# Performance work log

Hardware: AMD Instinct MI355X
Metric: run time of the kernel (lower is better)

## Reference

```python
import jax, jax.numpy as jnp
import numpy as np
from jax import lax

TAGSET = 32
START = 30  # tag_to_ix[START_TAG]
STOP = 31   # tag_to_ix[STOP_TAG]
# tag 0 is PAD

def setup_inputs() -> dict:
    key = jax.random.key(0)
    k1, k2, k3, k4 = jax.random.split(key, 4)
    B, L, T = 1024, 512, TAGSET
    feats = jax.random.normal(k1, (B, L, T), jnp.float32)
    transitions = jax.random.normal(k2, (T, T), jnp.float32) * 0.1
    word_seq_lens = jax.random.randint(k4, (B,), 1, L + 1)  # in [1, L]
    raw_tags = jax.random.randint(k3, (B, L), 1, 30)  # real tags in [1,30)
    pos = jnp.arange(L)[None, :]
    tags = jnp.where(pos < word_seq_lens[:, None], raw_tags, 0)  # PAD=0 beyond length
    return {"feats": feats, "transitions": transitions, "tags": tags,
            "word_seq_lens": word_seq_lens}


def _crf_nll(feats, transitions, tags, word_seq_lens):
    B, L, T = feats.shape

    # ---- forward algorithm (partition function), forward_pred ----
    # all_scores[b,l,i,j] = transitions[i,j] + feats[b,l,j]  (never materialized)
    alpha0 = transitions[START][None, :] + feats[:, 0]  # (B,T)

    def step(alpha, feat_t):
        # alpha:(B,T) over 'from' tag i; score[b,i,j] = alpha[b,i]+trans[i,j]+feat_t[b,j]
        m = alpha[:, :, None] + transitions[None, :, :] + feat_t[:, None, :]
        new = jax.nn.logsumexp(m, axis=1)  # (B,T)
        return new, new

    feats_t = jnp.swapaxes(feats, 0, 1)  # (L,B,T)
    _, alphas_rest = lax.scan(step, alpha0, feats_t[1:])
    alphas = jnp.concatenate([alpha0[None], alphas_rest], axis=0)  # (L,B,T)

    last_alpha = alphas[word_seq_lens - 1, jnp.arange(B)]  # (B,T) at position len-1
    last_alpha = last_alpha + transitions[:, STOP][None, :]
    forward_score = jnp.sum(jax.nn.logsumexp(last_alpha, axis=1))

    # ---- gold score, forward_labeled ----
    # currentTagScores[b,l,i] = transitions[i, tags[b,l]] + feats[b,l,tags[b,l]]
    emit = jnp.take_along_axis(feats, tags[:, :, None], axis=2)[:, :, 0]  # (B,L)
    cur = transitions.T[tags] + emit[:, :, None]  # (B,L,T)

    begin = cur[:, 0, START]  # (B,)
    end_tag = jnp.take_along_axis(tags, word_seq_lens[:, None] - 1, axis=1)[:, 0]
    end = transitions[end_tag, STOP]  # (B,)
    middle = jnp.take_along_axis(cur[:, 1:, :], tags[:, :L - 1, None], axis=2)[:, :, 0]
    mask = (tags[:, 1:] != 0).astype(feats.dtype)
    gold_score = jnp.sum(begin) + jnp.sum(end) + jnp.sum(middle * mask)

    return forward_score - gold_score


def reference(feats, transitions, tags, word_seq_lens):
    return _crf_nll(feats, transitions, tags, word_seq_lens)
```

## Files before the change

### kernel.cpp

```cpp
#include <hip/hip_runtime.h>

#define NTAG 32
#define START 30
#define STOP 31
#define LOG2E 1.44269504088896340736f
#define LN2 0.69314718055994530942f

typedef float f2 __attribute__((ext_vector_type(2)));
typedef float f4 __attribute__((ext_vector_type(4)));

__device__ __forceinline__ float fexp2(float x) {
#if __has_builtin(__builtin_amdgcn_exp2f)
    return __builtin_amdgcn_exp2f(x);
#else
    return exp2f(x);
#endif
}
__device__ __forceinline__ float flog2(float x) {
#if __has_builtin(__builtin_amdgcn_logf)
    return __builtin_amdgcn_logf(x);
#else
    return log2f(x);
#endif
}

#define PKMUL(d, s, e) asm("v_pk_mul_f32 %0, %1, %2" : "=v"(d) : "v"(s), "v"(e))
#define PKFMA(d, s, e) asm("v_pk_fma_f32 %0, %1, %2, %0" : "+v"(d) : "v"(s), "v"(e))
#define PKADD(d, x, y) asm("v_pk_add_f32 %0, %1, %2" : "=v"(d) : "v"(x), "v"(y))

#define REPEAT16(M) \
    M(0) M(1) M(2) M(3) M(4) M(5) M(6) M(7) \
    M(8) M(9) M(10) M(11) M(12) M(13) M(14) M(15)

#define STEP_CORE(fraw_, PRE, RN) { \
    const float F_ = fexp2((fraw_) * LOG2E); \
    const float y_ = (PRE) ? (S * F_) : S; \
    *swr = y_; \
    asm volatile("" ::: "memory"); \
    const f4 Q0 = srd4[0], Q1 = srd4[1], Q2 = srd4[2], Q3 = srd4[3], \
             Q4 = srd4[4], Q5 = srd4[5], Q6 = srd4[6], Q7 = srd4[7]; \
    const f2 s0  = __builtin_shufflevector(Q0, Q0, 0, 1), s1  = __builtin_shufflevector(Q0, Q0, 2, 3); \
    const f2 s2  = __builtin_shufflevector(Q1, Q1, 0, 1), s3  = __builtin_shufflevector(Q1, Q1, 2, 3); \
    const f2 s4  = __builtin_shufflevector(Q2, Q2, 0, 1), s5  = __builtin_shufflevector(Q2, Q2, 2, 3); \
    const f2 s6  = __builtin_shufflevector(Q3, Q3, 0, 1), s7  = __builtin_shufflevector(Q3, Q3, 2, 3); \
    const f2 s8  = __builtin_shufflevector(Q4, Q4, 0, 1), s9  = __builtin_shufflevector(Q4, Q4, 2, 3); \
    const f2 s10 = __builtin_shufflevector(Q5, Q5, 0, 1), s11 = __builtin_shufflevector(Q5, Q5, 2, 3); \
    const f2 s12 = __builtin_shufflevector(Q6, Q6, 0, 1), s13 = __builtin_shufflevector(Q6, Q6, 2, 3); \
    const f2 s14 = __builtin_shufflevector(Q7, Q7, 0, 1), s15 = __builtin_shufflevector(Q7, Q7, 2, 3); \
    f2 a0, a1, a2, a3; \
    PKMUL(a0, s0,  E2_0);  PKMUL(a1, s1,  E2_1);  PKMUL(a2, s2,  E2_2);  PKMUL(a3, s3,  E2_3); \
    PKFMA(a0, s4,  E2_4);  PKFMA(a1, s5,  E2_5);  PKFMA(a2, s6,  E2_6);  PKFMA(a3, s7,  E2_7); \
    PKFMA(a0, s8,  E2_8);  PKFMA(a1, s9,  E2_9);  PKFMA(a2, s10, E2_10); PKFMA(a3, s11, E2_11); \
    PKFMA(a0, s12, E2_12); PKFMA(a1, s13, E2_13); PKFMA(a2, s14, E2_14); PKFMA(a3, s15, E2_15); \
    f2 t01, t23, tt; \
    PKADD(t01, a0, a1); PKADD(t23, a2, a3); PKADD(tt, t01, t23); \
    const float r_ = tt.x + tt.y; \
    S = (PRE) ? r_ : (r_ * F_); \
    if (RN) { \
        const int k_ = ((__float_as_int(Q0.x) >> 23) & 0xff) - 127; \
        S = __int_as_float(__float_as_int(S) - (k_ << 23)); \
        M2i += k_; } }

#define STEP_RELOAD_F(FS, tload, RN) { const float fraw_ = FS; \
    { const int tc_ = ((tload) < L - 1) ? (tload) : (L - 1); \
      FS = frow[tc_ * NTAG + j]; } \
    STEP_CORE(fraw_, 0, RN) }
#define STEP_RELOAD_B(FS, tload, RN) { const float fraw_ = FS; \
    { const int tc_ = ((tload) > 0) ? (tload) : 0; \
      FS = frow[tc_ * NTAG + j]; } \
    STEP_CORE(fraw_, 1, RN) }

#define STEP_NR_F(FS, RN) { const float fraw_ = FS; STEP_CORE(fraw_, 0, RN) }
#define STEP_NR_B(FS, RN) { const float fraw_ = FS; STEP_CORE(fraw_, 1, RN) }

#define PIN_E2 \
    asm volatile("" : "+v"(E2_0),  "+v"(E2_1),  "+v"(E2_2),  "+v"(E2_3), \
                      "+v"(E2_4),  "+v"(E2_5),  "+v"(E2_6),  "+v"(E2_7)); \
    asm volatile("" : "+v"(E2_8),  "+v"(E2_9),  "+v"(E2_10), "+v"(E2_11), \
                      "+v"(E2_12), "+v"(E2_13), "+v"(E2_14), "+v"(E2_15));

__global__ __launch_bounds__(768, 1) void crf_nll_kernel(
    const float* __restrict__ feats,
    const float* __restrict__ trans,
    const int*   __restrict__ tags,
    const int*   __restrict__ wsl,
    float* __restrict__ out, int B, int L)
{
    __shared__ float strans[NTAG * NTAG];
    __shared__ __align__(16) float sBC[8][NTAG];
    __shared__ float sRes[8][NTAG];
    __shared__ int   sM2[8];
    for (int i = threadIdx.x; i < NTAG * NTAG; i += 768) strans[i] = trans[i];
    __syncthreads();

    const int wave = threadIdx.x >> 6;
    const int lane = threadIdx.x & 63;

    if (wave < 8) {
        const int dir = wave >> 2;
        int b = blockIdx.x * 4 + (wave & 3);
        if (b >= B) b = B - 1;
        b = __builtin_amdgcn_readfirstlane(b);
        if (lane < 32) {
            const int j = lane;
            const int n = __builtin_amdgcn_readfirstlane(wsl[b]);
            const int h = (n + 1) >> 1;
            const float* __restrict__ frow = feats + (size_t)b * L * NTAG;
            float* const swr = &sBC[wave][j];
            const f4* const srd4 = (const f4*)&sBC[wave][0];
            float S;
            int M2i = 0;

            if (dir == 0) {
#define DECL_E2(k) f2 E2_##k = { fexp2(strans[(2*(k)) * NTAG + j] * LOG2E), \
                                 fexp2(strans[(2*(k)+1) * NTAG + j] * LOG2E) };
                REPEAT16(DECL_E2)
#undef DECL_E2
                S = fexp2((strans[START * NTAG + j] + frow[j]) * LOG2E);
#define LDF(t_) frow[(((t_) < L - 1) ? (t_) : (L - 1)) * NTAG + j]
                float fA0 = LDF(1),  fA1 = LDF(2),  fA2 = LDF(3),  fA3 = LDF(4),
                      fA4 = LDF(5),  fA5 = LDF(6),  fA6 = LDF(7),  fA7 = LDF(8);
                float fB0 = LDF(9),  fB1 = LDF(10), fB2 = LDF(11), fB3 = LDF(12),
                      fB4 = LDF(13), fB5 = LDF(14), fB6 = LDF(15), fB7 = LDF(16);
#undef LDF
                int t = 1;
                for (; t + 16 <= h; t += 16) {
                    PIN_E2
                    STEP_RELOAD_F(fA0, t + 16, 0)
                    STEP_RELOAD_F(fA1, t + 17, 0)
                    STEP_RELOAD_F(fA2, t + 18, 0)
                    STEP_RELOAD_F(fA3, t + 19, 1)
                    STEP_RELOAD_F(fA4, t + 20, 0)
                    STEP_RELOAD_F(fA5, t + 21, 0)
                    STEP_RELOAD_F(fA6, t + 22, 0)
                    STEP_RELOAD_F(fA7, t + 23, 1)
                    STEP_RELOAD_F(fB0, t + 24, 0)
                    STEP_RELOAD_F(fB1, t + 25, 0)
                    STEP_RELOAD_F(fB2, t + 26, 0)
                    STEP_RELOAD_F(fB3, t + 27, 1)
                    STEP_RELOAD_F(fB4, t + 28, 0)
                    STEP_RELOAD_F(fB5, t + 29, 0)
                    STEP_RELOAD_F(fB6, t + 30, 0)
                    STEP_RELOAD_F(fB7, t + 31, 1)
                }
                if (t + 0  < h) { STEP_NR_F(fA0, 1) }
                if (t + 1  < h) { STEP_NR_F(fA1, 1) }
                if (t + 2  < h) { STEP_NR_F(fA2, 1) }
                if (t + 3  < h) { STEP_NR_F(fA3, 1) }
                if (t + 4  < h) { STEP_NR_F(fA4, 1) }
                if (t + 5  < h) { STEP_NR_F(fA5, 1) }
                if (t + 6  < h) { STEP_NR_F(fA6, 1) }
                if (t + 7  < h) { STEP_NR_F(fA7, 1) }
                if (t + 8  < h) { STEP_NR_F(fB0, 1) }
                if (t + 9  < h) { STEP_NR_F(fB1, 1) }
                if (t + 10 < h) { STEP_NR_F(fB2, 1) }
                if (t + 11 < h) { STEP_NR_F(fB3, 1) }
                if (t + 12 < h) { STEP_NR_F(fB4, 1) }
                if (t + 13 < h) { STEP_NR_F(fB5, 1) }
                if (t + 14 < h) { STEP_NR_F(fB6, 1) }
            } else {
#define DECL_E2(k) f2 E2_##k = { fexp2(strans[j * NTAG + (2*(k))] * LOG2E), \
                                 fexp2(strans[j * NTAG + (2*(k)+1)] * LOG2E) };
                REPEAT16(DECL_E2)
#undef DECL_E2
                S = fexp2(strans[j * NTAG + STOP] * LOG2E);
                const int cnt = n - h;
#define LDB(s_) frow[(((n - 1 - (s_)) > 0) ? (n - 1 - (s_)) : 0) * NTAG + j]
                float gA0 = LDB(0),  gA1 = LDB(1),  gA2 = LDB(2),  gA3 = LDB(3),
                      gA4 = LDB(4),  gA5 = LDB(5),  gA6 = LDB(6),  gA7 = LDB(7);
                float gB0 = LDB(8),  gB1 = LDB(9),  gB2 = LDB(10), gB3 = LDB(11),
                      gB4 = LDB(12), gB5 = LDB(13), gB6 = LDB(14), gB7 = LDB(15);
#undef LDB
                int s = 0;
                for (; s + 16 <= cnt; s += 16) {
                    PIN_E2
                    STEP_RELOAD_B(gA0, n - 1 - (s + 0)  - 16, 0)
                    STEP_RELOAD_B(gA1, n - 1 - (s + 1)  - 16, 0)
                    STEP_RELOAD_B(gA2, n - 1 - (s + 2)  - 16, 0)
                    STEP_RELOAD_B(gA3, n - 1 - (s + 3)  - 16, 1)
                    STEP_RELOAD_B(gA4, n - 1 - (s + 4)  - 16, 0)
                    STEP_RELOAD_B(gA5, n - 1 - (s + 5)  - 16, 0)
                    STEP_RELOAD_B(gA6, n - 1 - (s + 6)  - 16, 0)
                    STEP_RELOAD_B(gA7, n - 1 - (s + 7)  - 16, 1)
                    STEP_RELOAD_B(gB0, n - 1 - (s + 8)  - 16, 0)
                    STEP_RELOAD_B(gB1, n - 1 - (s + 9)  - 16, 0)
                    STEP_RELOAD_B(gB2, n - 1 - (s + 10) - 16, 0)
                    STEP_RELOAD_B(gB3, n - 1 - (s + 11) - 16, 1)
                    STEP_RELOAD_B(gB4, n - 1 - (s + 12) - 16, 0)
                    STEP_RELOAD_B(gB5, n - 1 - (s + 13) - 16, 0)
                    STEP_RELOAD_B(gB6, n - 1 - (s + 14) - 16, 0)
                    STEP_RELOAD_B(gB7, n - 1 - (s + 15) - 16, 1)
                }
                if (s + 0  < cnt) { STEP_NR_B(gA0, 1) }
                if (s + 1  < cnt) { STEP_NR_B(gA1, 1) }
                if (s + 2  < cnt) { STEP_NR_B(gA2, 1) }
                if (s + 3  < cnt) { STEP_NR_B(gA3, 1) }
                if (s + 4  < cnt) { STEP_NR_B(gA4, 1) }
                if (s + 5  < cnt) { STEP_NR_B(gA5, 1) }
                if (s + 6  < cnt) { STEP_NR_B(gA6, 1) }
                if (s + 7  < cnt) { STEP_NR_B(gA7, 1) }
                if (s + 8  < cnt) { STEP_NR_B(gB0, 1) }
                if (s + 9  < cnt) { STEP_NR_B(gB1, 1) }
                if (s + 10 < cnt) { STEP_NR_B(gB2, 1) }
                if (s + 11 < cnt) { STEP_NR_B(gB3, 1) }
                if (s + 12 < cnt) { STEP_NR_B(gB4, 1) }
                if (s + 13 < cnt) { STEP_NR_B(gB5, 1) }
                if (s + 14 < cnt) { STEP_NR_B(gB6, 1) }
            }
            sRes[wave][j] = S;
            if (j == 0) sM2[wave] = M2i;
        }
    } else {
        int b = blockIdx.x * 4 + (wave - 8);
        if (b < B) {
            b = __builtin_amdgcn_readfirstlane(b);
            const int n = wsl[b];
            const float* __restrict__ frow = feats + (size_t)b * L * NTAG;
            const int*   __restrict__ trow = tags  + (size_t)b * L;
            float acc = 0.f;
            for (int tt = lane; tt < L; tt += 64) {
                const int tg = trow[tt];
                if (tt == 0) {
                    acc += strans[START * NTAG + tg] + frow[tg];
                } else if (tt < n) {
                    const int tgp = trow[tt - 1];
                    acc += strans[tgp * NTAG + tg] + frow[tt * NTAG + tg];
                }
                if (tt == n - 1) {
                    acc += strans[tg * NTAG + STOP];
                }
            }
#pragma unroll
            for (int k = 1; k < 64; k <<= 1) acc += __shfl_xor(acc, k, 64);
            if (lane == 0) atomicAdd(out, -acc);
        }
    }

    __syncthreads();

    if (wave < 4) {
        const int b = blockIdx.x * 4 + wave;
        if (b < B && lane < 32) {
            float ex = sRes[wave][lane] * sRes[wave + 4][lane];
#pragma unroll
            for (int k = 1; k < 32; k <<= 1) ex += __shfl_xor(ex, k, 32);
            if (lane == 0)
                atomicAdd(out, LN2 * ((float)(sM2[wave] + sM2[wave + 4]) + flog2(ex)));
        }
    }
}

extern "C" void kernel_launch(void* const* d_in, const int* in_sizes, int n_in,
                              void* d_out, int out_size, void* d_ws, size_t ws_size,
                              hipStream_t stream) {
    const float* feats = (const float*)d_in[0];
    const float* trans = (const float*)d_in[1];
    const int*   tags  = (const int*)d_in[2];
    const int*   wsl   = (const int*)d_in[3];
    float* out = (float*)d_out;

    const int B = in_sizes[3];
    const int L = in_sizes[2] / B;

    (void)hipMemsetAsync(out, 0, sizeof(float), stream);
    const int grid = (B + 3) / 4;
    crf_nll_kernel<<<grid, 768, 0, stream>>>(feats, trans, tags, wsl, out, B, L);
}
```

Measured before the change: 139.2 us.

## Split CRF recurrence contraction across both wave halves using permlane32 swap

Each recurrence step now uses all 64 lanes of a wave. Each half-wave computes a partial dot product over 16 of the 32 source tags, and the two partials are combined with v_permlane32_swap. This halves the per-lane FMA chain and LDS read width, at the cost of an extra cross-lane swap per step. Renormalisation now uses each lane's own exponent, so per-lane scale counters are stored and rescaled to a common maximum in the final reduction.

New measurement: 129.8 us. 6.7% less time.

```diff
diff --git a/kernel.cpp b/kernel.cpp
--- a/kernel.cpp
+++ b/kernel.cpp
@@ -24,40 +24,45 @@
 #endif
 }
 
+__device__ __forceinline__ void plswap(float &a, float &b) {
+#if __has_builtin(__builtin_amdgcn_permlane32_swap)
+    auto r = __builtin_amdgcn_permlane32_swap(__float_as_int(a), __float_as_int(b),
+                                              false, false);
+    a = __int_as_float(r[0]);
+    b = __int_as_float(r[1]);
+#else
+    asm volatile("v_permlane32_swap_b32 %0, %1" : "+v"(a), "+v"(b));
+#endif
+}
+
 #define PKMUL(d, s, e) asm("v_pk_mul_f32 %0, %1, %2" : "=v"(d) : "v"(s), "v"(e))
 #define PKFMA(d, s, e) asm("v_pk_fma_f32 %0, %1, %2, %0" : "+v"(d) : "v"(s), "v"(e))
 #define PKADD(d, x, y) asm("v_pk_add_f32 %0, %1, %2" : "=v"(d) : "v"(x), "v"(y))
 
-#define REPEAT16(M) \
-    M(0) M(1) M(2) M(3) M(4) M(5) M(6) M(7) \
-    M(8) M(9) M(10) M(11) M(12) M(13) M(14) M(15)
+#define REPEAT8(M) M(0) M(1) M(2) M(3) M(4) M(5) M(6) M(7)
 
 #define STEP_CORE(fraw_, PRE, RN) { \
     const float F_ = fexp2((fraw_) * LOG2E); \
     const float y_ = (PRE) ? (S * F_) : S; \
     *swr = y_; \
     asm volatile("" ::: "memory"); \
-    const f4 Q0 = srd4[0], Q1 = srd4[1], Q2 = srd4[2], Q3 = srd4[3], \
-             Q4 = srd4[4], Q5 = srd4[5], Q6 = srd4[6], Q7 = srd4[7]; \
-    const f2 s0  = __builtin_shufflevector(Q0, Q0, 0, 1), s1  = __builtin_shufflevector(Q0, Q0, 2, 3); \
-    const f2 s2  = __builtin_shufflevector(Q1, Q1, 0, 1), s3  = __builtin_shufflevector(Q1, Q1, 2, 3); \
-    const f2 s4  = __builtin_shufflevector(Q2, Q2, 0, 1), s5  = __builtin_shufflevector(Q2, Q2, 2, 3); \
-    const f2 s6  = __builtin_shufflevector(Q3, Q3, 0, 1), s7  = __builtin_shufflevector(Q3, Q3, 2, 3); \
-    const f2 s8  = __builtin_shufflevector(Q4, Q4, 0, 1), s9  = __builtin_shufflevector(Q4, Q4, 2, 3); \
-    const f2 s10 = __builtin_shufflevector(Q5, Q5, 0, 1), s11 = __builtin_shufflevector(Q5, Q5, 2, 3); \
-    const f2 s12 = __builtin_shufflevector(Q6, Q6, 0, 1), s13 = __builtin_shufflevector(Q6, Q6, 2, 3); \
-    const f2 s14 = __builtin_shufflevector(Q7, Q7, 0, 1), s15 = __builtin_shufflevector(Q7, Q7, 2, 3); \
+    const f4 Q0 = srd4[0], Q1 = srd4[1], Q2 = srd4[2], Q3 = srd4[3]; \
+    const f2 s0 = __builtin_shufflevector(Q0, Q0, 0, 1), s1 = __builtin_shufflevector(Q0, Q0, 2, 3); \
+    const f2 s2 = __builtin_shufflevector(Q1, Q1, 0, 1), s3 = __builtin_shufflevector(Q1, Q1, 2, 3); \
+    const f2 s4 = __builtin_shufflevector(Q2, Q2, 0, 1), s5 = __builtin_shufflevector(Q2, Q2, 2, 3); \
+    const f2 s6 = __builtin_shufflevector(Q3, Q3, 0, 1), s7 = __builtin_shufflevector(Q3, Q3, 2, 3); \
     f2 a0, a1, a2, a3; \
-    PKMUL(a0, s0,  E2_0);  PKMUL(a1, s1,  E2_1);  PKMUL(a2, s2,  E2_2);  PKMUL(a3, s3,  E2_3); \
-    PKFMA(a0, s4,  E2_4);  PKFMA(a1, s5,  E2_5);  PKFMA(a2, s6,  E2_6);  PKFMA(a3, s7,  E2_7); \
-    PKFMA(a0, s8,  E2_8);  PKFMA(a1, s9,  E2_9);  PKFMA(a2, s10, E2_10); PKFMA(a3, s11, E2_11); \
-    PKFMA(a0, s12, E2_12); PKFMA(a1, s13, E2_13); PKFMA(a2, s14, E2_14); PKFMA(a3, s15, E2_15); \
+    PKMUL(a0, s0, E2_0); PKMUL(a1, s1, E2_1); PKMUL(a2, s2, E2_2); PKMUL(a3, s3, E2_3); \
+    PKFMA(a0, s4, E2_4); PKFMA(a1, s5, E2_5); PKFMA(a2, s6, E2_6); PKFMA(a3, s7, E2_7); \
     f2 t01, t23, tt; \
     PKADD(t01, a0, a1); PKADD(t23, a2, a3); PKADD(tt, t01, t23); \
-    const float r_ = tt.x + tt.y; \
+    const float part_ = tt.x + tt.y; \
+    float px_ = part_, py_ = part_; \
+    plswap(px_, py_); \
+    const float r_ = px_ + py_; \
     S = (PRE) ? r_ : (r_ * F_); \
     if (RN) { \
-        const int k_ = ((__float_as_int(Q0.x) >> 23) & 0xff) - 127; \
+        const int k_ = ((__float_as_int(S) >> 23) & 0xff) - 127; \
         S = __int_as_float(__float_as_int(S) - (k_ << 23)); \
         M2i += k_; } }
 
@@ -74,10 +79,8 @@
 #define STEP_NR_B(FS, RN) { const float fraw_ = FS; STEP_CORE(fraw_, 1, RN) }
 
 #define PIN_E2 \
-    asm volatile("" : "+v"(E2_0),  "+v"(E2_1),  "+v"(E2_2),  "+v"(E2_3), \
-                      "+v"(E2_4),  "+v"(E2_5),  "+v"(E2_6),  "+v"(E2_7)); \
-    asm volatile("" : "+v"(E2_8),  "+v"(E2_9),  "+v"(E2_10), "+v"(E2_11), \
-                      "+v"(E2_12), "+v"(E2_13), "+v"(E2_14), "+v"(E2_15));
+    asm volatile("" : "+v"(E2_0), "+v"(E2_1), "+v"(E2_2), "+v"(E2_3), \
+                      "+v"(E2_4), "+v"(E2_5), "+v"(E2_6), "+v"(E2_7));
 
 __global__ __launch_bounds__(768, 1) void crf_nll_kernel(
     const float* __restrict__ feats,
@@ -87,9 +90,9 @@
     float* __restrict__ out, int B, int L)
 {
     __shared__ float strans[NTAG * NTAG];
-    __shared__ __align__(16) float sBC[8][NTAG];
+    __shared__ __align__(16) float sBC[8][104];
     __shared__ float sRes[8][NTAG];
-    __shared__ int   sM2[8];
+    __shared__ int   sM2[8][NTAG];
     for (int i = threadIdx.x; i < NTAG * NTAG; i += 768) strans[i] = trans[i];
     __syncthreads();
 
@@ -101,115 +104,115 @@
         int b = blockIdx.x * 4 + (wave & 3);
         if (b >= B) b = B - 1;
         b = __builtin_amdgcn_readfirstlane(b);
-        if (lane < 32) {
-            const int j = lane;
-            const int n = __builtin_amdgcn_readfirstlane(wsl[b]);
-            const int h = (n + 1) >> 1;
-            const float* __restrict__ frow = feats + (size_t)b * L * NTAG;
-            float* const swr = &sBC[wave][j];
-            const f4* const srd4 = (const f4*)&sBC[wave][0];
-            float S;
-            int M2i = 0;
-
-            if (dir == 0) {
-#define DECL_E2(k) f2 E2_##k = { fexp2(strans[(2*(k)) * NTAG + j] * LOG2E), \
-                                 fexp2(strans[(2*(k)+1) * NTAG + j] * LOG2E) };
-                REPEAT16(DECL_E2)
+        const int j = lane & 31;
+        const bool up = lane >= 32;
+        const int ib = up ? 16 : 0;
+        const int n = __builtin_amdgcn_readfirstlane(wsl[b]);
+        const int h = (n + 1) >> 1;
+        const float* __restrict__ frow = feats + (size_t)b * L * NTAG;
+
+        float* const swr = &sBC[wave][(up ? 68 : 0) + j];
+        const f4* const srd4 = (const f4*)&sBC[wave][up ? 16 : 0];
+        float S;
+        int M2i = 0;
+
+        if (dir == 0) {
+#define DECL_E2(k) f2 E2_##k = { fexp2(strans[(ib + 2*(k)) * NTAG + j] * LOG2E), \
+                                 fexp2(strans[(ib + 2*(k) + 1) * NTAG + j] * LOG2E) };
+            REPEAT8(DECL_E2)
 #undef DECL_E2
-                S = fexp2((strans[START * NTAG + j] + frow[j]) * LOG2E);
+            S = fexp2((strans[START * NTAG + j] + frow[j]) * LOG2E);
 #define LDF(t_) frow[(((t_) < L - 1) ? (t_) : (L - 1)) * NTAG + j]
-                float fA0 = LDF(1),  fA1 = LDF(2),  fA2 = LDF(3),  fA3 = LDF(4),
-                      fA4 = LDF(5),  fA5 = LDF(6),  fA6 = LDF(7),  fA7 = LDF(8);
-                float fB0 = LDF(9),  fB1 = LDF(10), fB2 = LDF(11), fB3 = LDF(12),
-                      fB4 = LDF(13), fB5 = LDF(14), fB6 = LDF(15), fB7 = LDF(16);
+            float fA0 = LDF(1),  fA1 = LDF(2),  fA2 = LDF(3),  fA3 = LDF(4),
+                  fA4 = LDF(5),  fA5 = LDF(6),  fA6 = LDF(7),  fA7 = LDF(8);
+            float fB0 = LDF(9),  fB1 = LDF(10), fB2 = LDF(11), fB3 = LDF(12),
+                  fB4 = LDF(13), fB5 = LDF(14), fB6 = LDF(15), fB7 = LDF(16);
 #undef LDF
-                int t = 1;
-                for (; t + 16 <= h; t += 16) {
-                    PIN_E2
-                    STEP_RELOAD_F(fA0, t + 16, 0)
-                    STEP_RELOAD_F(fA1, t + 17, 0)
-                    STEP_RELOAD_F(fA2, t + 18, 0)
-                    STEP_RELOAD_F(fA3, t + 19, 1)
-                    STEP_RELOAD_F(fA4, t + 20, 0)
-                    STEP_RELOAD_F(fA5, t + 21, 0)
-                    STEP_RELOAD_F(fA6, t + 22, 0)
-                    STEP_RELOAD_F(fA7, t + 23, 1)
-                    STEP_RELOAD_F(fB0, t + 24, 0)
-                    STEP_RELOAD_F(fB1, t + 25, 0)
-                    STEP_RELOAD_F(fB2, t + 26, 0)
-                    STEP_RELOAD_F(fB3, t + 27, 1)
-                    STEP_RELOAD_F(fB4, t + 28, 0)
-                    STEP_RELOAD_F(fB5, t + 29, 0)
-                    STEP_RELOAD_F(fB6, t + 30, 0)
-                    STEP_RELOAD_F(fB7, t + 31, 1)
-                }
-                if (t + 0  < h) { STEP_NR_F(fA0, 1) }
-                if (t + 1  < h) { STEP_NR_F(fA1, 1) }
-                if (t + 2  < h) { STEP_NR_F(fA2, 1) }
-                if (t + 3  < h) { STEP_NR_F(fA3, 1) }
-                if (t + 4  < h) { STEP_NR_F(fA4, 1) }
-                if (t + 5  < h) { STEP_NR_F(fA5, 1) }
-                if (t + 6  < h) { STEP_NR_F(fA6, 1) }
-                if (t + 7  < h) { STEP_NR_F(fA7, 1) }
-                if (t + 8  < h) { STEP_NR_F(fB0, 1) }
-                if (t + 9  < h) { STEP_NR_F(fB1, 1) }
-                if (t + 10 < h) { STEP_NR_F(fB2, 1) }
-                if (t + 11 < h) { STEP_NR_F(fB3, 1) }
-                if (t + 12 < h) { STEP_NR_F(fB4, 1) }
-                if (t + 13 < h) { STEP_NR_F(fB5, 1) }
-                if (t + 14 < h) { STEP_NR_F(fB6, 1) }
-            } else {
-#define DECL_E2(k) f2 E2_##k = { fexp2(strans[j * NTAG + (2*(k))] * LOG2E), \
-                                 fexp2(strans[j * NTAG + (2*(k)+1)] * LOG2E) };
-                REPEAT16(DECL_E2)
+            int t = 1;
+            for (; t + 16 <= h; t += 16) {
+                PIN_E2
+                STEP_RELOAD_F(fA0, t + 16, 0)
+                STEP_RELOAD_F(fA1, t + 17, 0)
+                STEP_RELOAD_F(fA2, t + 18, 0)
+                STEP_RELOAD_F(fA3, t + 19, 1)
+                STEP_RELOAD_F(fA4, t + 20, 0)
+                STEP_RELOAD_F(fA5, t + 21, 0)
+                STEP_RELOAD_F(fA6, t + 22, 0)
+                STEP_RELOAD_F(fA7, t + 23, 1)
+                STEP_RELOAD_F(fB0, t + 24, 0)
+                STEP_RELOAD_F(fB1, t + 25, 0)
+                STEP_RELOAD_F(fB2, t + 26, 0)
+                STEP_RELOAD_F(fB3, t + 27, 1)
+                STEP_RELOAD_F(fB4, t + 28, 0)
+                STEP_RELOAD_F(fB5, t + 29, 0)
+                STEP_RELOAD_F(fB6, t + 30, 0)
+                STEP_RELOAD_F(fB7, t + 31, 1)
+            }
+            if (t + 0  < h) { STEP_NR_F(fA0, 1) }
+            if (t + 1  < h) { STEP_NR_F(fA1, 1) }
+            if (t + 2  < h) { STEP_NR_F(fA2, 1) }
+            if (t + 3  < h) { STEP_NR_F(fA3, 1) }
+            if (t + 4  < h) { STEP_NR_F(fA4, 1) }
+            if (t + 5  < h) { STEP_NR_F(fA5, 1) }
+            if (t + 6  < h) { STEP_NR_F(fA6, 1) }
+            if (t + 7  < h) { STEP_NR_F(fA7, 1) }
+            if (t + 8  < h) { STEP_NR_F(fB0, 1) }
+            if (t + 9  < h) { STEP_NR_F(fB1, 1) }
+            if (t + 10 < h) { STEP_NR_F(fB2, 1) }
+            if (t + 11 < h) { STEP_NR_F(fB3, 1) }
+            if (t + 12 < h) { STEP_NR_F(fB4, 1) }
+            if (t + 13 < h) { STEP_NR_F(fB5, 1) }
+            if (t + 14 < h) { STEP_NR_F(fB6, 1) }
+        } else {
+#define DECL_E2(k) f2 E2_##k = { fexp2(strans[j * NTAG + ib + 2*(k)] * LOG2E), \
+                                 fexp2(strans[j * NTAG + ib + 2*(k) + 1] * LOG2E) };
+            REPEAT8(DECL_E2)
 #undef DECL_E2
-                S = fexp2(strans[j * NTAG + STOP] * LOG2E);
-                const int cnt = n - h;
+            S = fexp2(strans[j * NTAG + STOP] * LOG2E);
+            const int cnt = n - h;
 #define LDB(s_) frow[(((n - 1 - (s_)) > 0) ? (n - 1 - (s_)) : 0) * NTAG + j]
-                float gA0 = LDB(0),  gA1 = LDB(1),  gA2 = LDB(2),  gA3 = LDB(3),
-                      gA4 = LDB(4),  gA5 = LDB(5),  gA6 = LDB(6),  gA7 = LDB(7);
-                float gB0 = LDB(8),  gB1 = LDB(9),  gB2 = LDB(10), gB3 = LDB(11),
-                      gB4 = LDB(12), gB5 = LDB(13), gB6 = LDB(14), gB7 = LDB(15);
+            float gA0 = LDB(0),  gA1 = LDB(1),  gA2 = LDB(2),  gA3 = LDB(3),
+                  gA4 = LDB(4),  gA5 = LDB(5),  gA6 = LDB(6),  gA7 = LDB(7);
+            float gB0 = LDB(8),  gB1 = LDB(9),  gB2 = LDB(10), gB3 = LDB(11),
+                  gB4 = LDB(12), gB5 = LDB(13), gB6 = LDB(14), gB7 = LDB(15);
 #undef LDB
-                int s = 0;
-                for (; s + 16 <= cnt; s += 16) {
-                    PIN_E2
-                    STEP_RELOAD_B(gA0, n - 1 - (s + 0)  - 16, 0)
-                    STEP_RELOAD_B(gA1, n - 1 - (s + 1)  - 16, 0)
-                    STEP_RELOAD_B(gA2, n - 1 - (s + 2)  - 16, 0)
-                    STEP_RELOAD_B(gA3, n - 1 - (s + 3)  - 16, 1)
-                    STEP_RELOAD_B(gA4, n - 1 - (s + 4)  - 16, 0)
-                    STEP_RELOAD_B(gA5, n - 1 - (s + 5)  - 16, 0)
-                    STEP_RELOAD_B(gA6, n - 1 - (s + 6)  - 16, 0)
-                    STEP_RELOAD_B(gA7, n - 1 - (s + 7)  - 16, 1)
-                    STEP_RELOAD_B(gB0, n - 1 - (s + 8)  - 16, 0)
-                    STEP_RELOAD_B(gB1, n - 1 - (s + 9)  - 16, 0)
-                    STEP_RELOAD_B(gB2, n - 1 - (s + 10) - 16, 0)
-                    STEP_RELOAD_B(gB3, n - 1 - (s + 11) - 16, 1)
-                    STEP_RELOAD_B(gB4, n - 1 - (s + 12) - 16, 0)
-                    STEP_RELOAD_B(gB5, n - 1 - (s + 13) - 16, 0)
-                    STEP_RELOAD_B(gB6, n - 1 - (s + 14) - 16, 0)
-                    STEP_RELOAD_B(gB7, n - 1 - (s + 15) - 16, 1)
-                }
-                if (s + 0  < cnt) { STEP_NR_B(gA0, 1) }
-                if (s + 1  < cnt) { STEP_NR_B(gA1, 1) }
-                if (s + 2  < cnt) { STEP_NR_B(gA2, 1) }
-                if (s + 3  < cnt) { STEP_NR_B(gA3, 1) }
-                if (s + 4  < cnt) { STEP_NR_B(gA4, 1) }
-                if (s + 5  < cnt) { STEP_NR_B(gA5, 1) }
-                if (s + 6  < cnt) { STEP_NR_B(gA6, 1) }
-                if (s + 7  < cnt) { STEP_NR_B(gA7, 1) }
-                if (s + 8  < cnt) { STEP_NR_B(gB0, 1) }
-                if (s + 9  < cnt) { STEP_NR_B(gB1, 1) }
-                if (s + 10 < cnt) { STEP_NR_B(gB2, 1) }
-                if (s + 11 < cnt) { STEP_NR_B(gB3, 1) }
-                if (s + 12 < cnt) { STEP_NR_B(gB4, 1) }
-                if (s + 13 < cnt) { STEP_NR_B(gB5, 1) }
-                if (s + 14 < cnt) { STEP_NR_B(gB6, 1) }
-            }
-            sRes[wave][j] = S;
-            if (j == 0) sM2[wave] = M2i;
+            int s = 0;
+            for (; s + 16 <= cnt; s += 16) {
+                PIN_E2
+                STEP_RELOAD_B(gA0, n - 1 - (s + 0)  - 16, 0)
+                STEP_RELOAD_B(gA1, n - 1 - (s + 1)  - 16, 0)
+                STEP_RELOAD_B(gA2, n - 1 - (s + 2)  - 16, 0)
+                STEP_RELOAD_B(gA3, n - 1 - (s + 3)  - 16, 1)
+                STEP_RELOAD_B(gA4, n - 1 - (s + 4)  - 16, 0)
+                STEP_RELOAD_B(gA5, n - 1 - (s + 5)  - 16, 0)
+                STEP_RELOAD_B(gA6, n - 1 - (s + 6)  - 16, 0)
+                STEP_RELOAD_B(gA7, n - 1 - (s + 7)  - 16, 1)
+                STEP_RELOAD_B(gB0, n - 1 - (s + 8)  - 16, 0)
+                STEP_RELOAD_B(gB1, n - 1 - (s + 9)  - 16, 0)
+                STEP_RELOAD_B(gB2, n - 1 - (s + 10) - 16, 0)
+                STEP_RELOAD_B(gB3, n - 1 - (s + 11) - 16, 1)
+                STEP_RELOAD_B(gB4, n - 1 - (s + 12) - 16, 0)
+                STEP_RELOAD_B(gB5, n - 1 - (s + 13) - 16, 0)
+                STEP_RELOAD_B(gB6, n - 1 - (s + 14) - 16, 0)
+                STEP_RELOAD_B(gB7, n - 1 - (s + 15) - 16, 1)
+            }
+            if (s + 0  < cnt) { STEP_NR_B(gA0, 1) }
+            if (s + 1  < cnt) { STEP_NR_B(gA1, 1) }
+            if (s + 2  < cnt) { STEP_NR_B(gA2, 1) }
+            if (s + 3  < cnt) { STEP_NR_B(gA3, 1) }
+            if (s + 4  < cnt) { STEP_NR_B(gA4, 1) }
+            if (s + 5  < cnt) { STEP_NR_B(gA5, 1) }
+            if (s + 6  < cnt) { STEP_NR_B(gA6, 1) }
+            if (s + 7  < cnt) { STEP_NR_B(gA7, 1) }
+            if (s + 8  < cnt) { STEP_NR_B(gB0, 1) }
+            if (s + 9  < cnt) { STEP_NR_B(gB1, 1) }
+            if (s + 10 < cnt) { STEP_NR_B(gB2, 1) }
+            if (s + 11 < cnt) { STEP_NR_B(gB3, 1) }
+            if (s + 12 < cnt) { STEP_NR_B(gB4, 1) }
+            if (s + 13 < cnt) { STEP_NR_B(gB5, 1) }
+            if (s + 14 < cnt) { STEP_NR_B(gB6, 1) }
         }
+        if (!up) { sRes[wave][j] = S; sM2[wave][j] = M2i; }
     } else {
         int b = blockIdx.x * 4 + (wave - 8);
         if (b < B) {
@@ -239,13 +242,21 @@
     __syncthreads();
 
     if (wave < 4) {
-        const int b = blockIdx.x * 4 + wave;
-        if (b < B && lane < 32) {
-            float ex = sRes[wave][lane] * sRes[wave + 4][lane];
+        const int b2 = blockIdx.x * 4 + wave;
+        if (b2 < B && lane < 32) {
+            const int M2s = sM2[wave][lane] + sM2[wave + 4][lane];
+            const float pr = sRes[wave][lane] * sRes[wave + 4][lane];
+            int mx = M2s;
+#pragma unroll
+            for (int k = 1; k < 32; k <<= 1) {
+                const int o = __shfl_xor(mx, k, 32);
+                mx = o > mx ? o : mx;
+            }
+            float ex = ldexpf(pr, M2s - mx);
 #pragma unroll
             for (int k = 1; k < 32; k <<= 1) ex += __shfl_xor(ex, k, 32);
             if (lane == 0)
-                atomicAdd(out, LN2 * ((float)(sM2[wave] + sM2[wave + 4]) + flog2(ex)));
+                atomicAdd(out, LN2 * ((float)mx + flog2(ex)));
         }
     }
 }
```

## Pack forward and backward CRF recursions into one wave's two half-waves

Applied to the files above, without the earlier changes.

The forward and backward CRF recursions for a sequence now run in the lower and upper 32 lanes of a single wave instead of two separate half-idle waves, so the block shrinks from 12 to 8 waves. The two halves are combined with a permlane32 swap plus shuffle reduction, which removes the trailing __syncthreads and shared-memory exchange. Loads now use a precomputed byte offset stepped each iteration, and the tail is a fixed 16-step predicated epilogue instead of branches. The forward and backward step counts can differ by one, so the main loop is bounded by the forward count and per-lane predication covers the rest, adding divergence-free but redundant work in the epilogue.

After: 139.7 us. No clear change (+0.4%).

```diff
diff --git a/kernel.cpp b/kernel.cpp
--- a/kernel.cpp
+++ b/kernel.cpp
@@ -24,6 +24,25 @@
 #endif
 }
 
+__device__ __forceinline__ void plswapf(float &a, float &b) {
+#if __has_builtin(__builtin_amdgcn_permlane32_swap)
+    auto r = __builtin_amdgcn_permlane32_swap(__float_as_int(a), __float_as_int(b),
+                                              false, false);
+    a = __int_as_float(r[0]);
+    b = __int_as_float(r[1]);
+#else
+    asm volatile("s_nop 1\n\tv_permlane32_swap_b32 %0, %1" : "+v"(a), "+v"(b));
+#endif
+}
+__device__ __forceinline__ void plswapi(int &a, int &b) {
+#if __has_builtin(__builtin_amdgcn_permlane32_swap)
+    auto r = __builtin_amdgcn_permlane32_swap(a, b, false, false);
+    a = r[0]; b = r[1];
+#else
+    asm volatile("s_nop 1\n\tv_permlane32_swap_b32 %0, %1" : "+v"(a), "+v"(b));
+#endif
+}
+
 #define PKMUL(d, s, e) asm("v_pk_mul_f32 %0, %1, %2" : "=v"(d) : "v"(s), "v"(e))
 #define PKFMA(d, s, e) asm("v_pk_fma_f32 %0, %1, %2, %0" : "+v"(d) : "v"(s), "v"(e))
 #define PKADD(d, x, y) asm("v_pk_add_f32 %0, %1, %2" : "=v"(d) : "v"(x), "v"(y))
@@ -32,9 +51,10 @@
     M(0) M(1) M(2) M(3) M(4) M(5) M(6) M(7) \
     M(8) M(9) M(10) M(11) M(12) M(13) M(14) M(15)
 
-#define STEP_CORE(fraw_, PRE, RN) { \
+#define STEP_CORE(fraw_, RN, ACT) { \
     const float F_ = fexp2((fraw_) * LOG2E); \
-    const float y_ = (PRE) ? (S * F_) : S; \
+    const float SF_ = S * F_; \
+    const float y_ = up ? SF_ : S; \
     *swr = y_; \
     asm volatile("" ::: "memory"); \
     const f4 Q0 = srd4[0], Q1 = srd4[1], Q2 = srd4[2], Q3 = srd4[3], \
@@ -55,23 +75,21 @@
     f2 t01, t23, tt; \
     PKADD(t01, a0, a1); PKADD(t23, a2, a3); PKADD(tt, t01, t23); \
     const float r_ = tt.x + tt.y; \
-    S = (PRE) ? r_ : (r_ * F_); \
+    const float rF_ = r_ * F_; \
+    const float val_ = up ? r_ : rF_; \
+    S = (ACT) ? val_ : S; \
     if (RN) { \
         const int k_ = ((__float_as_int(Q0.x) >> 23) & 0xff) - 127; \
         S = __int_as_float(__float_as_int(S) - (k_ << 23)); \
         M2i += k_; } }
 
-#define STEP_RELOAD_F(FS, tload, RN) { const float fraw_ = FS; \
-    { const int tc_ = ((tload) < L - 1) ? (tload) : (L - 1); \
-      FS = frow[tc_ * NTAG + j]; } \
-    STEP_CORE(fraw_, 0, RN) }
-#define STEP_RELOAD_B(FS, tload, RN) { const float fraw_ = FS; \
-    { const int tc_ = ((tload) > 0) ? (tload) : 0; \
-      FS = frow[tc_ * NTAG + j]; } \
-    STEP_CORE(fraw_, 1, RN) }
-
-#define STEP_NR_F(FS, RN) { const float fraw_ = FS; STEP_CORE(fraw_, 0, RN) }
-#define STEP_NR_B(FS, RN) { const float fraw_ = FS; STEP_CORE(fraw_, 1, RN) }
+#define STEP_RELOAD(FS, RN) { const float fraw_ = FS; \
+    { FS = *(const float*)((const char*)frow + (voff + d16)); voff += dStep; } \
+    STEP_CORE(fraw_, RN, 1) }
+
+#define STEP_EP(FS, i_) { const float fraw_ = FS; \
+    const bool act_ = (i_) < rl; \
+    STEP_CORE(fraw_, 1, act_) }
 
 #define PIN_E2 \
     asm volatile("" : "+v"(E2_0),  "+v"(E2_1),  "+v"(E2_2),  "+v"(E2_3), \
@@ -79,7 +97,7 @@
     asm volatile("" : "+v"(E2_8),  "+v"(E2_9),  "+v"(E2_10), "+v"(E2_11), \
                       "+v"(E2_12), "+v"(E2_13), "+v"(E2_14), "+v"(E2_15));
 
-__global__ __launch_bounds__(768, 1) void crf_nll_kernel(
+__global__ __launch_bounds__(512, 1) void crf_nll_kernel(
     const float* __restrict__ feats,
     const float* __restrict__ trans,
     const int*   __restrict__ tags,
@@ -87,131 +105,105 @@
     float* __restrict__ out, int B, int L)
 {
     __shared__ float strans[NTAG * NTAG];
-    __shared__ __align__(16) float sBC[8][NTAG];
-    __shared__ float sRes[8][NTAG];
-    __shared__ int   sM2[8];
-    for (int i = threadIdx.x; i < NTAG * NTAG; i += 768) strans[i] = trans[i];
+    __shared__ __align__(16) float sBC[4][2][NTAG];
+    for (int i = threadIdx.x; i < NTAG * NTAG; i += 512) strans[i] = trans[i];
     __syncthreads();
 
     const int wave = threadIdx.x >> 6;
     const int lane = threadIdx.x & 63;
 
-    if (wave < 8) {
-        const int dir = wave >> 2;
-        int b = blockIdx.x * 4 + (wave & 3);
-        if (b >= B) b = B - 1;
+    if (wave < 4) {
+        int b = blockIdx.x * 4 + wave;
+        const int bok = (b < B);
+        if (!bok) b = B - 1;
         b = __builtin_amdgcn_readfirstlane(b);
-        if (lane < 32) {
-            const int j = lane;
-            const int n = __builtin_amdgcn_readfirstlane(wsl[b]);
-            const int h = (n + 1) >> 1;
-            const float* __restrict__ frow = feats + (size_t)b * L * NTAG;
-            float* const swr = &sBC[wave][j];
-            const f4* const srd4 = (const f4*)&sBC[wave][0];
-            float S;
-            int M2i = 0;
-
-            if (dir == 0) {
-#define DECL_E2(k) f2 E2_##k = { fexp2(strans[(2*(k)) * NTAG + j] * LOG2E), \
-                                 fexp2(strans[(2*(k)+1) * NTAG + j] * LOG2E) };
-                REPEAT16(DECL_E2)
+
+        const int j = lane & 31;
+        const bool up = lane >= 32;
+        const int n = __builtin_amdgcn_readfirstlane(wsl[b]);
+        const int h = (n + 1) >> 1;
+        const int cf = h - 1;
+        const int cb = n - h;
+        const int climit = up ? cb : cf;
+        const float* __restrict__ frow = feats + (size_t)b * L * NTAG;
+
+#define DECL_E2(k) f2 E2_##k = { \
+        fexp2(strans[up ? (j * NTAG + 2*(k))     : ((2*(k)) * NTAG + j)]     * LOG2E), \
+        fexp2(strans[up ? (j * NTAG + 2*(k) + 1) : ((2*(k)+1) * NTAG + j)] * LOG2E) };
+        REPEAT16(DECL_E2)
 #undef DECL_E2
-                S = fexp2((strans[START * NTAG + j] + frow[j]) * LOG2E);
-#define LDF(t_) frow[(((t_) < L - 1) ? (t_) : (L - 1)) * NTAG + j]
-                float fA0 = LDF(1),  fA1 = LDF(2),  fA2 = LDF(3),  fA3 = LDF(4),
-                      fA4 = LDF(5),  fA5 = LDF(6),  fA6 = LDF(7),  fA7 = LDF(8);
-                float fB0 = LDF(9),  fB1 = LDF(10), fB2 = LDF(11), fB3 = LDF(12),
-                      fB4 = LDF(13), fB5 = LDF(14), fB6 = LDF(15), fB7 = LDF(16);
-#undef LDF
-                int t = 1;
-                for (; t + 16 <= h; t += 16) {
-                    PIN_E2
-                    STEP_RELOAD_F(fA0, t + 16, 0)
-                    STEP_RELOAD_F(fA1, t + 17, 0)
-                    STEP_RELOAD_F(fA2, t + 18, 0)
-                    STEP_RELOAD_F(fA3, t + 19, 1)
-                    STEP_RELOAD_F(fA4, t + 20, 0)
-                    STEP_RELOAD_F(fA5, t + 21, 0)
-                    STEP_RELOAD_F(fA6, t + 22, 0)
-                    STEP_RELOAD_F(fA7, t + 23, 1)
-                    STEP_RELOAD_F(fB0, t + 24, 0)
-                    STEP_RELOAD_F(fB1, t + 25, 0)
-                    STEP_RELOAD_F(fB2, t + 26, 0)
-                    STEP_RELOAD_F(fB3, t + 27, 1)
-                    STEP_RELOAD_F(fB4, t + 28, 0)
-                    STEP_RELOAD_F(fB5, t + 29, 0)
-                    STEP_RELOAD_F(fB6, t + 30, 0)
-                    STEP_RELOAD_F(fB7, t + 31, 1)
-                }
-                if (t + 0  < h) { STEP_NR_F(fA0, 1) }
-                if (t + 1  < h) { STEP_NR_F(fA1, 1) }
-                if (t + 2  < h) { STEP_NR_F(fA2, 1) }
-                if (t + 3  < h) { STEP_NR_F(fA3, 1) }
-                if (t + 4  < h) { STEP_NR_F(fA4, 1) }
-                if (t + 5  < h) { STEP_NR_F(fA5, 1) }
-                if (t + 6  < h) { STEP_NR_F(fA6, 1) }
-                if (t + 7  < h) { STEP_NR_F(fA7, 1) }
-                if (t + 8  < h) { STEP_NR_F(fB0, 1) }
-                if (t + 9  < h) { STEP_NR_F(fB1, 1) }
-                if (t + 10 < h) { STEP_NR_F(fB2, 1) }
-                if (t + 11 < h) { STEP_NR_F(fB3, 1) }
-                if (t + 12 < h) { STEP_NR_F(fB4, 1) }
-                if (t + 13 < h) { STEP_NR_F(fB5, 1) }
-                if (t + 14 < h) { STEP_NR_F(fB6, 1) }
-            } else {
-#define DECL_E2(k) f2 E2_##k = { fexp2(strans[j * NTAG + (2*(k))] * LOG2E), \
-                                 fexp2(strans[j * NTAG + (2*(k)+1)] * LOG2E) };
-                REPEAT16(DECL_E2)
-#undef DECL_E2
-                S = fexp2(strans[j * NTAG + STOP] * LOG2E);
-                const int cnt = n - h;
-#define LDB(s_) frow[(((n - 1 - (s_)) > 0) ? (n - 1 - (s_)) : 0) * NTAG + j]
-                float gA0 = LDB(0),  gA1 = LDB(1),  gA2 = LDB(2),  gA3 = LDB(3),
-                      gA4 = LDB(4),  gA5 = LDB(5),  gA6 = LDB(6),  gA7 = LDB(7);
-                float gB0 = LDB(8),  gB1 = LDB(9),  gB2 = LDB(10), gB3 = LDB(11),
-                      gB4 = LDB(12), gB5 = LDB(13), gB6 = LDB(14), gB7 = LDB(15);
-#undef LDB
-                int s = 0;
-                for (; s + 16 <= cnt; s += 16) {
-                    PIN_E2
-                    STEP_RELOAD_B(gA0, n - 1 - (s + 0)  - 16, 0)
-                    STEP_RELOAD_B(gA1, n - 1 - (s + 1)  - 16, 0)
-                    STEP_RELOAD_B(gA2, n - 1 - (s + 2)  - 16, 0)
-                    STEP_RELOAD_B(gA3, n - 1 - (s + 3)  - 16, 1)
-                    STEP_RELOAD_B(gA4, n - 1 - (s + 4)  - 16, 0)
-                    STEP_RELOAD_B(gA5, n - 1 - (s + 5)  - 16, 0)
-                    STEP_RELOAD_B(gA6, n - 1 - (s + 6)  - 16, 0)
-                    STEP_RELOAD_B(gA7, n - 1 - (s + 7)  - 16, 1)
-                    STEP_RELOAD_B(gB0, n - 1 - (s + 8)  - 16, 0)
-                    STEP_RELOAD_B(gB1, n - 1 - (s + 9)  - 16, 0)
-                    STEP_RELOAD_B(gB2, n - 1 - (s + 10) - 16, 0)
-                    STEP_RELOAD_B(gB3, n - 1 - (s + 11) - 16, 1)
-                    STEP_RELOAD_B(gB4, n - 1 - (s + 12) - 16, 0)
-                    STEP_RELOAD_B(gB5, n - 1 - (s + 13) - 16, 0)
-                    STEP_RELOAD_B(gB6, n - 1 - (s + 14) - 16, 0)
-                    STEP_RELOAD_B(gB7, n - 1 - (s + 15) - 16, 1)
-                }
-                if (s + 0  < cnt) { STEP_NR_B(gA0, 1) }
-                if (s + 1  < cnt) { STEP_NR_B(gA1, 1) }
-                if (s + 2  < cnt) { STEP_NR_B(gA2, 1) }
-                if (s + 3  < cnt) { STEP_NR_B(gA3, 1) }
-                if (s + 4  < cnt) { STEP_NR_B(gA4, 1) }
-                if (s + 5  < cnt) { STEP_NR_B(gA5, 1) }
-                if (s + 6  < cnt) { STEP_NR_B(gA6, 1) }
-                if (s + 7  < cnt) { STEP_NR_B(gA7, 1) }
-                if (s + 8  < cnt) { STEP_NR_B(gB0, 1) }
-                if (s + 9  < cnt) { STEP_NR_B(gB1, 1) }
-                if (s + 10 < cnt) { STEP_NR_B(gB2, 1) }
-                if (s + 11 < cnt) { STEP_NR_B(gB3, 1) }
-                if (s + 12 < cnt) { STEP_NR_B(gB4, 1) }
-                if (s + 13 < cnt) { STEP_NR_B(gB5, 1) }
-                if (s + 14 < cnt) { STEP_NR_B(gB6, 1) }
-            }
-            sRes[wave][j] = S;
-            if (j == 0) sM2[wave] = M2i;
+
+        const float s0v = up ? strans[j * NTAG + STOP]
+                             : (strans[START * NTAG + j] + frow[j]);
+        float S = fexp2(s0v * LOG2E);
+        int M2i = 0;
+
+        float* const swr = &sBC[wave][up][j];
+        const f4* const srd4 = (const f4*)&sBC[wave][up][0];
+
+        int voff = ((up ? (n - 1) : 1) * NTAG + j) * 4;
+        const int dStep = up ? -(NTAG * 4) : (NTAG * 4);
+        const int d16 = dStep * 16;
+
+#define LDI(i_) frow[(up ? ((n - 1 - (i_)) > 0 ? (n - 1 - (i_)) : 0) : (1 + (i_))) * NTAG + j]
+        float fA0 = LDI(0),  fA1 = LDI(1),  fA2 = LDI(2),  fA3 = LDI(3),
+              fA4 = LDI(4),  fA5 = LDI(5),  fA6 = LDI(6),  fA7 = LDI(7);
+        float fB0 = LDI(8),  fB1 = LDI(9),  fB2 = LDI(10), fB3 = LDI(11),
+              fB4 = LDI(12), fB5 = LDI(13), fB6 = LDI(14), fB7 = LDI(15);
+#undef LDI
+
+        int c = 0;
+        for (; c + 16 <= cf; c += 16) {
+            PIN_E2
+            STEP_RELOAD(fA0, 0)
+            STEP_RELOAD(fA1, 0)
+            STEP_RELOAD(fA2, 0)
+            STEP_RELOAD(fA3, 1)
+            STEP_RELOAD(fA4, 0)
+            STEP_RELOAD(fA5, 0)
+            STEP_RELOAD(fA6, 0)
+            STEP_RELOAD(fA7, 1)
+            STEP_RELOAD(fB0, 0)
+            STEP_RELOAD(fB1, 0)
+            STEP_RELOAD(fB2, 0)
+            STEP_RELOAD(fB3, 1)
+            STEP_RELOAD(fB4, 0)
+            STEP_RELOAD(fB5, 0)
+            STEP_RELOAD(fB6, 0)
+            STEP_RELOAD(fB7, 1)
         }
+        {
+            const int rl = climit - c;
+            STEP_EP(fA0, 0)
+            STEP_EP(fA1, 1)
+            STEP_EP(fA2, 2)
+            STEP_EP(fA3, 3)
+            STEP_EP(fA4, 4)
+            STEP_EP(fA5, 5)
+            STEP_EP(fA6, 6)
+            STEP_EP(fA7, 7)
+            STEP_EP(fB0, 8)
+            STEP_EP(fB1, 9)
+            STEP_EP(fB2, 10)
+            STEP_EP(fB3, 11)
+            STEP_EP(fB4, 12)
+            STEP_EP(fB5, 13)
+            STEP_EP(fB6, 14)
+            STEP_EP(fB7, 15)
+        }
+
+        float pa = S, pb = S;
+        plswapf(pa, pb);
+        float prod = pa * pb;
+#pragma unroll
+        for (int k = 1; k < 32; k <<= 1) prod += __shfl_xor(prod, k, 32);
+        int ma = M2i, mb = M2i;
+        plswapi(ma, mb);
+        const int M2tot = ma + mb;
+        if (lane == 0 && bok)
+            atomicAdd(out, LN2 * ((float)M2tot + flog2(prod)));
     } else {
-        int b = blockIdx.x * 4 + (wave - 8);
+        int b = blockIdx.x * 4 + (wave - 4);
         if (b < B) {
             b = __builtin_amdgcn_readfirstlane(b);
             const int n = wsl[b];
@@ -235,19 +227,6 @@
             if (lane == 0) atomicAdd(out, -acc);
         }
     }
-
-    __syncthreads();
-
-    if (wave < 4) {
-        const int b = blockIdx.x * 4 + wave;
-        if (b < B && lane < 32) {
-            float ex = sRes[wave][lane] * sRes[wave + 4][lane];
-#pragma unroll
-            for (int k = 1; k < 32; k <<= 1) ex += __shfl_xor(ex, k, 32);
-            if (lane == 0)
-                atomicAdd(out, LN2 * ((float)(sM2[wave] + sM2[wave + 4]) + flog2(ex)));
-        }
-    }
 }
 
 extern "C" void kernel_launch(void* const* d_in, const int* in_sizes, int n_in,
@@ -264,5 +243,5 @@
 
     (void)hipMemsetAsync(out, 0, sizeof(float), stream);
     const int grid = (B + 3) / 4;
-    crf_nll_kernel<<<grid, 768, 0, stream>>>(feats, trans, tags, wsl, out, B, L);
-}
+    crf_nll_kernel<<<grid, 512, 0, stream>>>(feats, trans, tags, wsl, out, B, L);
+}
```
